# Performance work log

Measured on AMD Instinct MI355X. Metric: run time of the kernel, lower is better.

## Reference

```python
import jax, jax.numpy as jnp
import numpy as np

N_CLASSES = 64
MAX_ITER = 50
EPS = 1e-4


def _sqdist(x, y):
    # squared euclidean distances [n, m]
    d = (x * x).sum(-1)[:, None] + (y * y).sum(-1)[None, :] - 2.0 * (x @ y.T)
    return jnp.maximum(d, 0.0)


def setup_inputs() -> dict:
    key = jax.random.key(0)
    k1, k2, k3 = jax.random.split(key, 3)
    return {
        "feat_s": jax.random.normal(k1, (1600, 1024), jnp.float32),
        "y_s": jax.random.randint(k2, (1600,), 0, N_CLASSES),
        "feat_q": jax.random.normal(k3, (4096, 1024), jnp.float32),
    }


def _prototypes(feat_s, y_s):
    sums = jax.ops.segment_sum(feat_s, y_s, num_segments=N_CLASSES)
    cnt = jax.ops.segment_sum(jnp.ones((feat_s.shape[0],), feat_s.dtype), y_s, num_segments=N_CLASSES)
    return sums / jnp.maximum(cnt, 1.0)[:, None]


def _affinity(feat):
    n = feat.shape[0]
    k = max(1, int(np.log2(n)))  # self-tuning neighborhood size
    dist = jnp.sqrt(_sqdist(feat, feat))
    _, nn_idx = jax.lax.top_k(-dist, k + 1)  # ascending distance order
    rows = jnp.arange(n)
    sigma = dist[rows, nn_idx[:, k]] + 1e-8  # k-th neighbor distance
    nbrs = nn_idx[:, 1:]  # [n, k], drop self
    w = jnp.exp(-jnp.take_along_axis(dist, nbrs, axis=1) / (sigma[:, None] * sigma[nbrs]))
    W = jnp.zeros((n, n), feat.dtype).at[rows[:, None], nbrs].set(w)
    W = (W + W.T) / 2.0
    D_inv = 1.0 / (W.sum(1) + 1e-8)
    return W, D_inv


def _mm_iterations(feat, prototypes, W, D_inv, lam):
    a = _sqdist(feat, prototypes)  # [n, C]
    coef = (lam * D_inv)[:, None]

    def step(y):
        return jax.nn.softmax(-a + coef * (W @ y), axis=1)

    y0 = jax.nn.softmax(-a, axis=1)

    def cond(s):
        y, y_new, i = s
        return (i < MAX_ITER) & (jnp.max(jnp.abs(y_new - y)) >= EPS)

    def body(s):
        y, y_new, i = s
        return (y_new, step(y_new), i + 1)

    y, _, _ = jax.lax.while_loop(cond, body, (y0, step(y0), 0))
    return y


def reference(feat_s, y_s, feat_q):
    protos = _prototypes(feat_s, y_s)
    W, D_inv = _affinity(feat_q)
    d2 = _sqdist(feat_q, protos).min(1)  # squared min distance to prototypes
    d = jnp.sqrt(d2)
    lam = jnp.exp(-d2 / (2.0 * jnp.median(d) ** 2 + 1e-8))
    y = _mm_iterations(feat_q, protos, W, D_inv, lam)
    return jnp.argmax(y, axis=1)
```

## Files before the change

kernel.cpp:

```cpp
#include <hip/hip_runtime.h>
#include <hip/hip_cooperative_groups.h>
#include <cfloat>
#include <cmath>

#define N_Q 4096
#define N_S 1600
#define DIM 1024
#define N_C 64
#define KNN 12
#define MAX_ITER 50
#define EPS_CONV 1e-4f
#define NBLK 256
#define ADJ_CAP 96
#define CHK 256
#define DPAD 40

typedef _Float16 h8 __attribute__((ext_vector_type(8)));
typedef float    f4 __attribute__((ext_vector_type(4)));

__device__ __forceinline__ float wave_max64(float v){
  #pragma unroll
  for (int o = 32; o; o >>= 1) v = fmaxf(v, __shfl_xor(v, o, 64));
  return v;
}
__device__ __forceinline__ float wave_sum64(float v){
  #pragma unroll
  for (int o = 32; o; o >>= 1) v += __shfl_xor(v, o, 64);
  return v;
}
__device__ __forceinline__ float wave_min64(float v){
  #pragma unroll
  for (int o = 32; o; o >>= 1) v = fminf(v, __shfl_xor(v, o, 64));
  return v;
}

__device__ __forceinline__ float aload(const float* p){
  return __hip_atomic_load(p, __ATOMIC_RELAXED, __HIP_MEMORY_SCOPE_AGENT);
}
__device__ __forceinline__ void astore(float* p, float v){
  __hip_atomic_store(p, v, __ATOMIC_RELAXED, __HIP_MEMORY_SCOPE_AGENT);
}
__device__ __forceinline__ int aloadi(const int* p){
  return __hip_atomic_load(p, __ATOMIC_RELAXED, __HIP_MEMORY_SCOPE_AGENT);
}
__device__ __forceinline__ void astorei(int* p, int v){
  __hip_atomic_store(p, v, __ATOMIC_RELAXED, __HIP_MEMORY_SCOPE_AGENT);
}
__device__ __forceinline__ unsigned long long aload64(const unsigned long long* p){
  return __hip_atomic_load(p, __ATOMIC_RELAXED, __HIP_MEMORY_SCOPE_AGENT);
}
__device__ __forceinline__ void astore64(unsigned long long* p, unsigned long long v){
  __hip_atomic_store(p, v, __ATOMIC_RELAXED, __HIP_MEMORY_SCOPE_AGENT);
}

__global__ __launch_bounds__(256) void proto_kernel(
    const float* __restrict__ fs, const int* __restrict__ ys,
    float* __restrict__ Pt, float* __restrict__ pn)
{
  const int c = blockIdx.x, t = threadIdx.x;
  __shared__ int list[N_S];
  __shared__ int pref[256];
  __shared__ int lcount;

  int loc[7]; int cnt = 0;
  const int base = t * 7;
  #pragma unroll
  for (int u = 0; u < 7; u++){
    const int i = base + u;
    if (i < N_S && ys[i] == c) loc[cnt++] = i;
  }
  pref[t] = cnt;
  __syncthreads();
  for (int off = 1; off < 256; off <<= 1){
    int v = (t >= off) ? pref[t - off] : 0;
    __syncthreads();
    pref[t] += v;
    __syncthreads();
  }
  const int start = pref[t] - cnt;
  for (int u = 0; u < cnt; u++) list[start + u] = loc[u];
  if (t == 255) lcount = pref[255];
  __syncthreads();

  const int n = lcount;
  float a0 = 0.f, a1 = 0.f, a2 = 0.f, a3 = 0.f;
  for (int m = 0; m < n; m++){
    const float* r = fs + (size_t)list[m] * DIM;
    a0 += r[t]; a1 += r[t + 256]; a2 += r[t + 512]; a3 += r[t + 768];
  }
  const float inv = 1.0f / fmaxf((float)n, 1.0f);
  const float v0 = a0*inv, v1 = a1*inv, v2 = a2*inv, v3 = a3*inv;
  Pt[(t      )*N_C + c] = v0;
  Pt[(t + 256)*N_C + c] = v1;
  Pt[(t + 512)*N_C + c] = v2;
  Pt[(t + 768)*N_C + c] = v3;
  __shared__ float red[256];
  red[t] = v0*v0 + v1*v1 + v2*v2 + v3*v3;
  __syncthreads();
  for (int o = 128; o; o >>= 1){ if (t < o) red[t] += red[t + o]; __syncthreads(); }
  if (t == 0) pn[c] = red[0];
}

__global__ __launch_bounds__(256) void prep_kernel(
    const float* __restrict__ X, float* __restrict__ qn,
    _Float16* __restrict__ Xh, _Float16* __restrict__ Xl)
{
  const int i = blockIdx.x, t = threadIdx.x;
  const float* r = X + (size_t)i * DIM;
  const float v0 = r[t], v1 = r[t+256], v2 = r[t+512], v3 = r[t+768];
  const size_t b = (size_t)i * DIM;
  _Float16 h0 = (_Float16)v0, h1 = (_Float16)v1, h2 = (_Float16)v2, h3 = (_Float16)v3;
  Xh[b + t      ] = h0; Xl[b + t      ] = (_Float16)(v0 - (float)h0);
  Xh[b + t + 256] = h1; Xl[b + t + 256] = (_Float16)(v1 - (float)h1);
  Xh[b + t + 512] = h2; Xl[b + t + 512] = (_Float16)(v2 - (float)h2);
  Xh[b + t + 768] = h3; Xl[b + t + 768] = (_Float16)(v3 - (float)h3);
  __shared__ float red[256];
  red[t] = v0*v0 + v1*v1 + v2*v2 + v3*v3;
  __syncthreads();
  for (int o = 128; o; o >>= 1){ if (t < o) red[t] += red[t + o]; __syncthreads(); }
  if (t == 0) qn[i] = red[0];
}

__global__ __launch_bounds__(256, 3) void dist_mfma(
    const _Float16* __restrict__ Xh, const _Float16* __restrict__ Xl,
    const float* __restrict__ qn, float* __restrict__ Dq)
{
  __shared__ __align__(16) _Float16 As[2][128][DPAD];
  __shared__ __align__(16) _Float16 Bs[2][128][DPAD];

  const int t = threadIdx.x, w = t >> 6, l = t & 63;
  const int lb  = blockIdx.y * 32 + blockIdx.x;
  const int xcd = lb & 7, k = lb >> 3;
  const int bxs = xcd * 4 + (k >> 5);
  const int bys = k & 31;
  const int bi0 = bys * 128, bj0 = bxs * 128;
  const int i0w = (w >> 1) * 64;
  const int j0w = (w & 1) * 64;
  const int fr = l & 15;
  const int kq = (l >> 4) * 8;

  const int srow = t >> 1;
  const int sseg = (t & 1) * 16;

  f4 acc[4][4];
  #pragma unroll
  for (int a = 0; a < 4; a++)
    #pragma unroll
    for (int b = 0; b < 4; b++) acc[a][b] = (f4){0.f, 0.f, 0.f, 0.f};

  const size_t abase = (size_t)(bi0 + srow) * DIM + sseg;
  const size_t bbase = (size_t)(bj0 + srow) * DIM + sseg;

  #pragma unroll 1
  for (int k0 = 0; k0 < DIM; k0 += 32){
    h8 va0 = *(const h8*)(Xh + abase + k0);
    h8 va1 = *(const h8*)(Xh + abase + k0 + 8);
    h8 vb0 = *(const h8*)(Xl + abase + k0);
    h8 vb1 = *(const h8*)(Xl + abase + k0 + 8);
    h8 vc0 = *(const h8*)(Xh + bbase + k0);
    h8 vc1 = *(const h8*)(Xh + bbase + k0 + 8);
    h8 vd0 = *(const h8*)(Xl + bbase + k0);
    h8 vd1 = *(const h8*)(Xl + bbase + k0 + 8);
    __syncthreads();
    *(h8*)&As[0][srow][sseg    ] = va0;
    *(h8*)&As[0][srow][sseg + 8] = va1;
    *(h8*)&As[1][srow][sseg    ] = vb0;
    *(h8*)&As[1][srow][sseg + 8] = vb1;
    *(h8*)&Bs[0][srow][sseg    ] = vc0;
    *(h8*)&Bs[0][srow][sseg + 8] = vc1;
    *(h8*)&Bs[1][srow][sseg    ] = vd0;
    *(h8*)&Bs[1][srow][sseg + 8] = vd1;
    __syncthreads();

    h8 ah[4], al[4];
    #pragma unroll
    for (int sm = 0; sm < 4; sm++){
      ah[sm] = *(const h8*)&As[0][i0w + sm * 16 + fr][kq];
      al[sm] = *(const h8*)&As[1][i0w + sm * 16 + fr][kq];
    }
    #pragma unroll
    for (int sn = 0; sn < 4; sn++){
      h8 bh = *(const h8*)&Bs[0][j0w + sn * 16 + fr][kq];
      h8 bl = *(const h8*)&Bs[1][j0w + sn * 16 + fr][kq];
      #pragma unroll
      for (int sm = 0; sm < 4; sm++){
        acc[sm][sn] = __builtin_amdgcn_mfma_f32_16x16x32_f16(ah[sm], bh, acc[sm][sn], 0, 0, 0);
        acc[sm][sn] = __builtin_amdgcn_mfma_f32_16x16x32_f16(ah[sm], bl, acc[sm][sn], 0, 0, 0);
        acc[sm][sn] = __builtin_amdgcn_mfma_f32_16x16x32_f16(al[sm], bh, acc[sm][sn], 0, 0, 0);
      }
    }
  }

  const int i0 = bi0 + i0w;
  const int j0 = bj0 + j0w;
  const int cr = (l >> 4) * 4;
  const int cc = l & 15;
  #pragma unroll
  for (int sm = 0; sm < 4; sm++){
    #pragma unroll
    for (int r = 0; r < 4; r++){
      const int row = i0 + sm * 16 + cr + r;
      const float qi = qn[row];
      float* dstrow = &Dq[(size_t)row * N_Q];
      #pragma unroll
      for (int sn = 0; sn < 4; sn++){
        const int col = j0 + sn * 16 + cc;
        float d2 = qi + qn[col] - 2.0f * acc[sm][sn][r];
        dstrow[col] = sqrtf(fmaxf(d2, 0.f));
      }
    }
  }
}

__global__ __launch_bounds__(256) void topk_kernel(
    const float* __restrict__ Dq, int* __restrict__ nbr,
    float* __restrict__ dnbr, float* __restrict__ sigma)
{
  const int i = blockIdx.x, t = threadIdx.x;
  const float* row = Dq + (size_t)i * N_Q;
  float r[16];
  #pragma unroll
  for (int u = 0; u < 16; u++) r[u] = row[t + u * 256];

  __shared__ float pvf[4];
  __shared__ int   pif[4];
  __shared__ int   bwi_s;

  for (int s = 0; s < KNN + 1; s++){
    float best = FLT_MAX; int bj = 0x7fffffff;
    #pragma unroll
    for (int u = 0; u < 16; u++){
      float v = r[u];
      if (v < best){ best = v; bj = t + u * 256; }
    }
    #pragma unroll
    for (int o = 32; o; o >>= 1){
      float ov = __shfl_xor(best, o, 64); int oj = __shfl_xor(bj, o, 64);
      if (ov < best || (ov == best && oj < bj)){ best = ov; bj = oj; }
    }
    if ((t & 63) == 0){ pvf[t >> 6] = best; pif[t >> 6] = bj; }
    __syncthreads();
    if (t == 0){
      float bv = pvf[0]; int bi2 = pif[0];
      #pragma unroll
      for (int w2 = 1; w2 < 4; w2++){
        float v2 = pvf[w2]; int i2 = pif[w2];
        if (v2 < bv || (v2 == bv && i2 < bi2)){ bv = v2; bi2 = i2; }
      }
      bwi_s = bi2;
      if (s >= 1){ nbr[i*KNN + s - 1] = bi2; dnbr[i*KNN + s - 1] = bv; }
      if (s == KNN) sigma[i] = bv + 1e-8f;
    }
    __syncthreads();
    const int widx = bwi_s;
    if ((widx & 255) == t) r[widx >> 8] = FLT_MAX;
  }
}

__device__ __forceinline__ void gbar_leader(int* garr, int* gcnt, int* gen, int target){
  const int g = blockIdx.x >> 4;
  int old = __hip_atomic_fetch_add(&garr[g * 32], 1, __ATOMIC_RELAXED, __HIP_MEMORY_SCOPE_AGENT);
  if ((old & 15) == 15){
    int o2 = __hip_atomic_fetch_add(gcnt, 1, __ATOMIC_RELAXED, __HIP_MEMORY_SCOPE_AGENT);
    if ((o2 & 15) == 15)
      __hip_atomic_fetch_add(gen, 1, __ATOMIC_RELAXED, __HIP_MEMORY_SCOPE_AGENT);
  }
  while (__hip_atomic_load(gen, __ATOMIC_RELAXED, __HIP_MEMORY_SCOPE_AGENT) < target)
    __builtin_amdgcn_s_sleep(1);
}

__device__ __forceinline__ void pbar_wave0(
    unsigned long long* pslot, int ph, int* sdm, float* sdelta_sh, int lane)
{
  const int par = ph & 1;
  unsigned long long* base = pslot + (size_t)par * NBLK;
  if (lane == 0){
    int myd = sdm[par]; sdm[par] = 0;
    unsigned long long pack =
        ((unsigned long long)(unsigned int)myd << 32) | (unsigned int)ph;
    __builtin_amdgcn_s_waitcnt(0);
    astore64(&base[blockIdx.x], pack);
  }
  int mx;
  while (1){
    unsigned long long v0 = aload64(&base[lane      ]);
    unsigned long long v1 = aload64(&base[lane +  64]);
    unsigned long long v2 = aload64(&base[lane + 128]);
    unsigned long long v3 = aload64(&base[lane + 192]);
    int f0 = (int)(unsigned int)v0, f1 = (int)(unsigned int)v1;
    int f2 = (int)(unsigned int)v2, f3 = (int)(unsigned int)v3;
    int mn = f0 < f1 ? f0 : f1;
    mn = f2 < mn ? f2 : mn;
    mn = f3 < mn ? f3 : mn;
    if (__all(mn >= ph)){
      int d0 = (int)(v0 >> 32), d1 = (int)(v1 >> 32);
      int d2 = (int)(v2 >> 32), d3 = (int)(v3 >> 32);
      mx = d0 > d1 ? d0 : d1;
      mx = d2 > mx ? d2 : mx;
      mx = d3 > mx ? d3 : mx;
      break;
    }
    __builtin_amdgcn_s_sleep(1);
  }
  #pragma unroll
  for (int o = 32; o; o >>= 1){ int ox = __shfl_xor(mx, o, 64); mx = ox > mx ? ox : mx; }
  if (lane == 0) *sdelta_sh = __int_as_float(mx);
}

template<int K>
__device__ __forceinline__ void chunk_fma(
    const float* __restrict__ src, const int2* adj, int gbase, int lane,
    float& s0, float& s1, float& s2, float& s3,
    float& s4, float& s5, float& s6, float& s7)
{
  float yv[K][8], wv[K][8];
  #pragma unroll
  for (int g = 0; g < K; g++){
    #pragma unroll
    for (int u = 0; u < 8; u++){
      int2 a = adj[(gbase + g) * 8 + u];
      wv[g][u] = __int_as_float(a.y);
      yv[g][u] = aload(&src[a.x + lane]);
    }
  }
  #pragma unroll
  for (int g = 0; g < K; g++){
    s0 = fmaf(wv[g][0], yv[g][0], s0);
    s1 = fmaf(wv[g][1], yv[g][1], s1);
    s2 = fmaf(wv[g][2], yv[g][2], s2);
    s3 = fmaf(wv[g][3], yv[g][3], s3);
    s4 = fmaf(wv[g][4], yv[g][4], s4);
    s5 = fmaf(wv[g][5], yv[g][5], s5);
    s6 = fmaf(wv[g][6], yv[g][6], s6);
    s7 = fmaf(wv[g][7], yv[g][7], s7);
  }
}

__device__ __forceinline__ float spmv_row(
    const float* __restrict__ src, const int2* adj,
    const int* __restrict__ colA, const float* __restrict__ wA,
    int p0, int p1v, int lane)
{
  const int deg  = p1v - p0;
  const int ncap = deg < ADJ_CAP ? deg : ADJ_CAP;
  const int nfull = ncap & ~7;
  const int ng = nfull >> 3;
  float s0=0.f,s1=0.f,s2=0.f,s3=0.f,s4=0.f,s5=0.f,s6=0.f,s7=0.f;

  int g = 0;
  #pragma unroll 1
  for (; g + 4 <= ng; g += 4){
    chunk_fma<4>(src, adj, g, lane, s0,s1,s2,s3,s4,s5,s6,s7);
  }
  {
    const int left = ng - g;
    if (left == 3)      chunk_fma<3>(src, adj, g, lane, s0,s1,s2,s3,s4,s5,s6,s7);
    else if (left == 2) chunk_fma<2>(src, adj, g, lane, s0,s1,s2,s3,s4,s5,s6,s7);
    else if (left == 1) chunk_fma<1>(src, adj, g, lane, s0,s1,s2,s3,s4,s5,s6,s7);
  }

  if (deg > ADJ_CAP){
    int qg = p0 + ADJ_CAP;
    for (; qg + 8 <= p1v; qg += 8){
      s0 = fmaf(wA[qg    ], aload(&src[colA[qg    ] + lane]), s0);
      s1 = fmaf(wA[qg + 1], aload(&src[colA[qg + 1] + lane]), s1);
      s2 = fmaf(wA[qg + 2], aload(&src[colA[qg + 2] + lane]), s2);
      s3 = fmaf(wA[qg + 3], aload(&src[colA[qg + 3] + lane]), s3);
      s4 = fmaf(wA[qg + 4], aload(&src[colA[qg + 4] + lane]), s4);
      s5 = fmaf(wA[qg + 5], aload(&src[colA[qg + 5] + lane]), s5);
      s6 = fmaf(wA[qg + 6], aload(&src[colA[qg + 6] + lane]), s6);
      s7 = fmaf(wA[qg + 7], aload(&src[colA[qg + 7] + lane]), s7);
    }
    for (; qg < p1v; qg++)
      s0 = fmaf(wA[qg], aload(&src[colA[qg] + lane]), s0);
  } else {
    const int rem = deg - nfull;
    if (rem > 0){
      float yr[7], wr[7];
      #pragma unroll
      for (int u = 0; u < 7; u++){
        if (u < rem){
          int2 a = adj[nfull + u];
          wr[u] = __int_as_float(a.y);
          yr[u] = aload(&src[a.x + lane]);
        }
      }
      #pragma unroll
      for (int u = 0; u < 7; u++)
        if (u < rem) s0 = fmaf(wr[u], yr[u], s0);
    }
  }
  return ((s0+s1)+(s2+s3)) + ((s4+s5)+(s6+s7));
}

__global__ __launch_bounds__(1024, 4) void tail_loop(
    const float* __restrict__ Xq, const float* __restrict__ Pt,
    const float* __restrict__ pn, const float* __restrict__ qn,
    const int* __restrict__ nbr, const float* __restrict__ dnbr,
    const float* __restrict__ sigma,
    float* d2min, float* denom, float* wh,
    float* rowsum, int* indeg, int* rowptr, int* fillc,
    int* colA, float* wA, float* buf0, float* buf1,
    unsigned long long* pslot,
    int* gcnt, int* gen, int* garr, int* __restrict__ out)
{
  __shared__ int   sdm[2];
  __shared__ float sdelta;
  __shared__ union {
    float pchunk[CHK * N_C];
    struct {
      int   ipart[1024];
      int   hist[1024];
      float cand[4096];
      int   candn, b1s, b2s;
    } s;
  } U;
  __shared__ int2  adjL[16 * ADJ_CAP];

  const int tid  = threadIdx.x;
  const int lane = tid & 63;
  const int wv   = tid >> 6;
  const int row  = blockIdx.x * 16 + wv;
  if (tid == 0){ sdm[0] = 0; sdm[1] = 0; }

  const float* xr = Xq + (size_t)row * DIM;
  const f4*    xr4 = (const f4*)xr;
  float dp[8];
  #pragma unroll
  for (int u = 0; u < 8; u++) dp[u] = 0.f;

  for (int f0 = 0; f0 < DIM; f0 += CHK){
    const f4* srcv = (const f4*)(Pt + (size_t)f0 * N_C);
    f4* dstv = (f4*)U.pchunk;
    #pragma unroll
    for (int u = 0; u < 4; u++) dstv[tid + u * 1024] = srcv[tid + u * 1024];
    __syncthreads();
    #pragma unroll 1
    for (int f = 0; f < CHK; f += 8){
      const f4 xa = xr4[(f0 + f) >> 2];
      const f4 xb = xr4[((f0 + f) >> 2) + 1];
      const float* pc = U.pchunk + f * N_C + lane;
      dp[0] = fmaf(xa[0], pc[0      ], dp[0]);
      dp[1] = fmaf(xa[1], pc[N_C    ], dp[1]);
      dp[2] = fmaf(xa[2], pc[N_C * 2], dp[2]);
      dp[3] = fmaf(xa[3], pc[N_C * 3], dp[3]);
      dp[4] = fmaf(xb[0], pc[N_C * 4], dp[4]);
      dp[5] = fmaf(xb[1], pc[N_C * 5], dp[5]);
      dp[6] = fmaf(xb[2], pc[N_C * 6], dp[6]);
      dp[7] = fmaf(xb[3], pc[N_C * 7], dp[7]);
    }
    __syncthreads();
  }
  const float dot = ((dp[0]+dp[1])+(dp[2]+dp[3])) + ((dp[4]+dp[5])+(dp[6]+dp[7]));
  const float av  = fmaxf(qn[row] + pn[lane] - 2.0f * dot, 0.0f);
  const float d2m = wave_min64(av);
  if (lane == 0) astore(&d2min[row], d2m);

  const int e = blockIdx.x * 1024 + tid;
  if (e < N_Q * KNN){
    const int i = e / KNN;
    const int j = nbr[e];
    float wgt = 0.5f * expf(-dnbr[e] / (sigma[i] * sigma[j]));
    astore(&wh[e], wgt);
    atomicAdd(&rowsum[i], wgt);
    atomicAdd(&rowsum[j], wgt);
    atomicAdd(&indeg[j], 1);
  }

  __syncthreads();
  if (tid == 0) gbar_leader(garr, gcnt, gen, 1);
  __syncthreads();

  float xv = -av;
  float m = wave_max64(xv), ee = expf(xv - m), ss = wave_sum64(ee);
  float prev = ee / ss;
  astore(&buf0[row * N_C + lane], prev);

  if (blockIdx.x == 0){
    int* ipart = U.s.ipart;
    const int base = tid * 4;
    int c0 = aloadi(&indeg[base]),     c1 = aloadi(&indeg[base + 1]);
    int c2 = aloadi(&indeg[base + 2]), c3 = aloadi(&indeg[base + 3]);
    const int s4 = c0 + c1 + c2 + c3;
    ipart[tid] = s4;
    __syncthreads();
    for (int off = 1; off < 1024; off <<= 1){
      int v = (tid >= off) ? ipart[tid - off] : 0;
      __syncthreads();
      ipart[tid] += v;
      __syncthreads();
    }
    int run = ipart[tid] - s4;
    astorei(&rowptr[base    ], KNN * (base    ) + run); run += c0;
    astorei(&rowptr[base + 1], KNN * (base + 1) + run); run += c1;
    astorei(&rowptr[base + 2], KNN * (base + 2) + run); run += c2;
    astorei(&rowptr[base + 3], KNN * (base + 3) + run);
    if (tid == 1023) astorei(&rowptr[N_Q], KNN * N_Q + ipart[1023]);
  }
  if (blockIdx.x == 1){
    int*   hist = U.s.hist;
    float* cand = U.s.cand;
    const int base = tid * 4;
    float dv[4];
    #pragma unroll
    for (int u = 0; u < 4; u++) dv[u] = sqrtf(aload(&d2min[base + u]));
    float mn = fminf(fminf(dv[0], dv[1]), fminf(dv[2], dv[3]));
    float mx = fmaxf(fmaxf(dv[0], dv[1]), fmaxf(dv[2], dv[3]));
    mn = wave_min64(mn); mx = wave_max64(mx);
    if (lane == 0){ cand[wv] = mn; cand[wv + 16] = mx; }
    __syncthreads();
    if (tid == 0){
      float a = cand[0], b = cand[16];
      for (int k = 1; k < 16; k++){ a = fminf(a, cand[k]); b = fmaxf(b, cand[16 + k]); }
      cand[32] = a; cand[33] = b;
    }
    __syncthreads();
    mn = cand[32]; mx = cand[33];
    const float rng = mx - mn;
    const float scale = (rng > 0.f) ? (1024.0f / rng) : 0.f;
    hist[tid] = 0;
    __syncthreads();
    int bidx[4];
    #pragma unroll
    for (int u = 0; u < 4; u++){
      int b = (int)((dv[u] - mn) * scale);
      b = b < 0 ? 0 : (b > 1023 ? 1023 : b);
      bidx[u] = b;
      atomicAdd(&hist[b], 1);
    }
    __syncthreads();
    for (int off = 1; off < 1024; off <<= 1){
      int v = (tid >= off) ? hist[tid - off] : 0;
      __syncthreads();
      hist[tid] += v;
      __syncthreads();
    }
    if (hist[tid] >= 2048 && (tid == 0 || hist[tid - 1] < 2048)) U.s.b1s = tid;
    if (hist[tid] >= 2049 && (tid == 0 || hist[tid - 1] < 2049)) U.s.b2s = tid;
    if (tid == 0) U.s.candn = 0;
    __syncthreads();
    const int b1 = U.s.b1s, b2 = U.s.b2s;
    const int cntBefore = (b1 > 0) ? hist[b1 - 1] : 0;
    #pragma unroll
    for (int u = 0; u < 4; u++){
      if (bidx[u] >= b1 && bidx[u] <= b2){
        int pos = atomicAdd(&U.s.candn, 1);
        cand[pos] = dv[u];
      }
    }
    __syncthreads();
    const int mcnt = U.s.candn;
    int P = 2; while (P < mcnt) P <<= 1;
    for (int i2 = mcnt + tid; i2 < P; i2 += 1024) cand[i2] = FLT_MAX;
    __syncthreads();
    for (int k = 2; k <= P; k <<= 1){
      for (int st = k >> 1; st > 0; st >>= 1){
        for (int i2 = tid; i2 < P; i2 += 1024){
          int j2 = i2 ^ st;
          if (j2 > i2){
            float a2 = cand[i2], b3 = cand[j2];
            bool up = ((i2 & k) == 0);
            if (up ? (a2 > b3) : (a2 < b3)){ cand[i2] = b3; cand[j2] = a2; }
          }
        }
        __syncthreads();
      }
    }
    if (tid == 0){
      float v1 = cand[2047 - cntBefore], v2 = cand[2048 - cntBefore];
      float med = 0.5f * (v1 + v2);
      astore(denom, 2.0f * med * med + 1e-8f);
    }
  }

  __syncthreads();
  if (tid == 0) gbar_leader(garr, gcnt, gen, 2);
  __syncthreads();

  if (e < N_Q * KNN){
    const int i = e / KNN, tt = e % KNN;
    const int j = nbr[e];
    const float wgt = aload(&wh[e]);
    const int p = aloadi(&rowptr[i]) + tt;
    colA[p] = j * N_C; wA[p] = wgt;
    const int q = aloadi(&rowptr[j]) + KNN + atomicAdd(&fillc[j], 1);
    colA[q] = i * N_C; wA[q] = wgt;
  }
  const float cf = expf(-d2m / aload(denom)) / (aload(&rowsum[row]) + 1e-8f);
  const int p0  = aloadi(&rowptr[row]);
  const int p1v = aloadi(&rowptr[row + 1]);

  __builtin_amdgcn_fence(__ATOMIC_RELEASE, "agent");
  __syncthreads();
  if (tid == 0) gbar_leader(garr, gcnt, gen, 3);
  __syncthreads();
  __builtin_amdgcn_fence(__ATOMIC_ACQUIRE, "agent");

  {
    const int deg  = p1v - p0;
    const int ncap = deg < ADJ_CAP ? deg : ADJ_CAP;
    for (int u = lane; u < ncap; u += 64)
      adjL[wv * ADJ_CAP + u] = make_int2(colA[p0 + u], __float_as_int(wA[p0 + u]));
  }
  __syncthreads();
  const int2* adj = adjL + wv * ADJ_CAP;

  float cur;
  {
    float sum = spmv_row(buf0, adj, colA, wA, p0, p1v, lane);
    float xv2 = -av + cf * sum;
    float mm = wave_max64(xv2), e2 = expf(xv2 - mm), ss2 = wave_sum64(e2);
    cur = e2 / ss2;
    astore(&buf1[row * N_C + lane], cur);
  }
  float dm = wave_max64(fabsf(cur - prev));
  if (lane == 0) atomicMax(&sdm[1], __float_as_int(dm));
  __syncthreads();
  if (wv == 0) pbar_wave0(pslot, 1, sdm, &sdelta, lane);
  __syncthreads();
  float delta = sdelta;

  int par = 1;
  for (int t = 0;; t++){
    if (t >= MAX_ITER || delta < EPS_CONV) break;
    const float* src = par ? buf1 : buf0;
    float*       dst = par ? buf0 : buf1;
    float sum = spmv_row(src, adj, colA, wA, p0, p1v, lane);
    float xv2 = -av + cf * sum;
    float mm = wave_max64(xv2), e2 = expf(xv2 - mm), ss2 = wave_sum64(e2);
    float nxt = e2 / ss2;
    astore(&dst[row * N_C + lane], nxt);
    const int ph = t + 2;
    dm = wave_max64(fabsf(nxt - cur));
    if (lane == 0) atomicMax(&sdm[ph & 1], __float_as_int(dm));
    __syncthreads();
    if (wv == 0) pbar_wave0(pslot, ph, sdm, &sdelta, lane);
    __syncthreads();
    delta = sdelta;
    prev = cur; cur = nxt; par ^= 1;
  }

  float bv = prev; int bi = lane;
  #pragma unroll
  for (int o = 32; o; o >>= 1){
    float ov = __shfl_xor(bv, o, 64); int oi = __shfl_xor(bi, o, 64);
    if (ov > bv || (ov == bv && oi < bi)){ bv = ov; bi = oi; }
  }
  if (lane == 0) out[row] = bi;
}

extern "C" void kernel_launch(void* const* d_in, const int* in_sizes, int n_in,
                              void* d_out, int out_size, void* d_ws, size_t ws_size,
                              hipStream_t stream)
{
  const float* feat_s = (const float*)d_in[0];
  const int*   y_s    = (const int*)d_in[1];
  const float* feat_q = (const float*)d_in[2];
  int* out = (int*)d_out;

  char* wp = (char*)d_ws;
  auto alloc = [&](size_t bytes) -> char* {
    char* p = wp;
    wp += (bytes + 255) & ~(size_t)255;
    return p;
  };
  float*     Dq  = (float*)alloc((size_t)N_Q * N_Q * 4);
  _Float16*  Xh  = (_Float16*)alloc((size_t)N_Q * DIM * 2);
  _Float16*  Xl  = (_Float16*)alloc((size_t)N_Q * DIM * 2);
  float* Pt     = (float*)alloc((size_t)DIM * N_C * 4);
  float* pn     = (float*)alloc(N_C * 4);
  float* qn     = (float*)alloc(N_Q * 4);
  float* d2min  = (float*)alloc(N_Q * 4);
  float* denom  = (float*)alloc(256);
  int*   nbr    = (int*)alloc((size_t)N_Q * KNN * 4);
  float* dnbr   = (float*)alloc((size_t)N_Q * KNN * 4);
  float* sigma  = (float*)alloc(N_Q * 4);
  float* wh     = (float*)alloc((size_t)N_Q * KNN * 4);
  int*   rowptr = (int*)alloc((N_Q + 1) * 4);
  int*   colA   = (int*)alloc((size_t)2 * N_Q * KNN * 4);
  float* wA     = (float*)alloc((size_t)2 * N_Q * KNN * 4);
  float* buf0   = (float*)alloc((size_t)N_Q * N_C * 4);
  float* buf1   = (float*)alloc((size_t)N_Q * N_C * 4);
  const size_t zbytes = (size_t)N_Q*12 + 256 + 2048 + 2 * NBLK * 8;
  char*  zbase  = alloc(zbytes);
  float* rowsum = (float*)(zbase);
  int*   indeg  = (int*)(zbase + N_Q*4);
  int*   fillc  = (int*)(zbase + N_Q*8);
  int*   syncw  = (int*)(zbase + N_Q*12);
  int*   garr   = (int*)(zbase + N_Q*12 + 256);
  unsigned long long* pslot = (unsigned long long*)(zbase + N_Q*12 + 256 + 2048);

  hipMemsetAsync(zbase, 0, zbytes, stream);

  proto_kernel <<<N_C, 256, 0, stream>>>(feat_s, y_s, Pt, pn);
  prep_kernel  <<<N_Q, 256, 0, stream>>>(feat_q, qn, Xh, Xl);
  dist_mfma    <<<dim3(N_Q/128, N_Q/128), 256, 0, stream>>>(Xh, Xl, qn, Dq);
  topk_kernel  <<<N_Q, 256, 0, stream>>>(Dq, nbr, dnbr, sigma);

  int* gcnt = &syncw[0];
  int* gen  = &syncw[32];
  const float* Xq = feat_q;
  void* args[] = {&Xq, &Pt, &pn, &qn, &nbr, &dnbr, &sigma,
                  &d2min, &denom, &wh, &rowsum, &indeg, &rowptr, &fillc,
                  &colA, &wA, &buf0, &buf1, &pslot,
                  &gcnt, &gen, &garr, &out};
  hipLaunchCooperativeKernel((void*)tail_loop, dim3(NBLK), dim3(1024), args, 0, stream);
}
```

Before: 476.3 us.

## Merge prototype and prep kernels; make top-k selection per-wave without block barriers

Combines the prototype-averaging and query fp16 split/norm kernels into one launch, indexing blocks by role, to remove a launch and let both run concurrently. Rewrites the top-k kernel so each wave independently extracts its own 13 smallest candidates using only shuffles, then one wave merges the 4x13 candidates. This removes the per-step __syncthreads and shared-memory round trips from the 13-step selection loop. The cost is extra candidate storage and a serial merge in a single wave.

```diff
diff --git a/kernel.cpp b/kernel.cpp
--- a/kernel.cpp
+++ b/kernel.cpp
@@ -53,72 +53,77 @@
   __hip_atomic_store(p, v, __ATOMIC_RELAXED, __HIP_MEMORY_SCOPE_AGENT);
 }
 
-__global__ __launch_bounds__(256) void proto_kernel(
+__global__ __launch_bounds__(256) void setup_kernel(
     const float* __restrict__ fs, const int* __restrict__ ys,
-    float* __restrict__ Pt, float* __restrict__ pn)
-{
-  const int c = blockIdx.x, t = threadIdx.x;
-  __shared__ int list[N_S];
-  __shared__ int pref[256];
-  __shared__ int lcount;
-
-  int loc[7]; int cnt = 0;
-  const int base = t * 7;
-  #pragma unroll
-  for (int u = 0; u < 7; u++){
-    const int i = base + u;
-    if (i < N_S && ys[i] == c) loc[cnt++] = i;
-  }
-  pref[t] = cnt;
-  __syncthreads();
-  for (int off = 1; off < 256; off <<= 1){
-    int v = (t >= off) ? pref[t - off] : 0;
-    __syncthreads();
-    pref[t] += v;
-    __syncthreads();
-  }
-  const int start = pref[t] - cnt;
-  for (int u = 0; u < cnt; u++) list[start + u] = loc[u];
-  if (t == 255) lcount = pref[255];
-  __syncthreads();
-
-  const int n = lcount;
-  float a0 = 0.f, a1 = 0.f, a2 = 0.f, a3 = 0.f;
-  for (int m = 0; m < n; m++){
-    const float* r = fs + (size_t)list[m] * DIM;
-    a0 += r[t]; a1 += r[t + 256]; a2 += r[t + 512]; a3 += r[t + 768];
-  }
-  const float inv = 1.0f / fmaxf((float)n, 1.0f);
-  const float v0 = a0*inv, v1 = a1*inv, v2 = a2*inv, v3 = a3*inv;
-  Pt[(t      )*N_C + c] = v0;
-  Pt[(t + 256)*N_C + c] = v1;
-  Pt[(t + 512)*N_C + c] = v2;
-  Pt[(t + 768)*N_C + c] = v3;
-  __shared__ float red[256];
-  red[t] = v0*v0 + v1*v1 + v2*v2 + v3*v3;
-  __syncthreads();
-  for (int o = 128; o; o >>= 1){ if (t < o) red[t] += red[t + o]; __syncthreads(); }
-  if (t == 0) pn[c] = red[0];
-}
-
-__global__ __launch_bounds__(256) void prep_kernel(
+    float* __restrict__ Pt, float* __restrict__ pn,
     const float* __restrict__ X, float* __restrict__ qn,
     _Float16* __restrict__ Xh, _Float16* __restrict__ Xl)
 {
-  const int i = blockIdx.x, t = threadIdx.x;
-  const float* r = X + (size_t)i * DIM;
-  const float v0 = r[t], v1 = r[t+256], v2 = r[t+512], v3 = r[t+768];
-  const size_t b = (size_t)i * DIM;
-  _Float16 h0 = (_Float16)v0, h1 = (_Float16)v1, h2 = (_Float16)v2, h3 = (_Float16)v3;
-  Xh[b + t      ] = h0; Xl[b + t      ] = (_Float16)(v0 - (float)h0);
-  Xh[b + t + 256] = h1; Xl[b + t + 256] = (_Float16)(v1 - (float)h1);
-  Xh[b + t + 512] = h2; Xl[b + t + 512] = (_Float16)(v2 - (float)h2);
-  Xh[b + t + 768] = h3; Xl[b + t + 768] = (_Float16)(v3 - (float)h3);
-  __shared__ float red[256];
-  red[t] = v0*v0 + v1*v1 + v2*v2 + v3*v3;
-  __syncthreads();
-  for (int o = 128; o; o >>= 1){ if (t < o) red[t] += red[t + o]; __syncthreads(); }
-  if (t == 0) qn[i] = red[0];
+  __shared__ union {
+    struct {
+      int   list[N_S];
+      int   pref[256];
+      int   lcount;
+      float red[256];
+    } p;
+    float red[256];
+  } S;
+
+  const int t = threadIdx.x;
+
+  if (blockIdx.x < N_C){
+    const int c = blockIdx.x;
+    int loc[7]; int cnt = 0;
+    const int base = t * 7;
+    #pragma unroll
+    for (int u = 0; u < 7; u++){
+      const int i = base + u;
+      if (i < N_S && ys[i] == c) loc[cnt++] = i;
+    }
+    S.p.pref[t] = cnt;
+    __syncthreads();
+    for (int off = 1; off < 256; off <<= 1){
+      int v = (t >= off) ? S.p.pref[t - off] : 0;
+      __syncthreads();
+      S.p.pref[t] += v;
+      __syncthreads();
+    }
+    const int start = S.p.pref[t] - cnt;
+    for (int u = 0; u < cnt; u++) S.p.list[start + u] = loc[u];
+    if (t == 255) S.p.lcount = S.p.pref[255];
+    __syncthreads();
+
+    const int n = S.p.lcount;
+    float a0 = 0.f, a1 = 0.f, a2 = 0.f, a3 = 0.f;
+    for (int m = 0; m < n; m++){
+      const float* r = fs + (size_t)S.p.list[m] * DIM;
+      a0 += r[t]; a1 += r[t + 256]; a2 += r[t + 512]; a3 += r[t + 768];
+    }
+    const float inv = 1.0f / fmaxf((float)n, 1.0f);
+    const float v0 = a0*inv, v1 = a1*inv, v2 = a2*inv, v3 = a3*inv;
+    Pt[(t      )*N_C + c] = v0;
+    Pt[(t + 256)*N_C + c] = v1;
+    Pt[(t + 512)*N_C + c] = v2;
+    Pt[(t + 768)*N_C + c] = v3;
+    S.p.red[t] = v0*v0 + v1*v1 + v2*v2 + v3*v3;
+    __syncthreads();
+    for (int o = 128; o; o >>= 1){ if (t < o) S.p.red[t] += S.p.red[t + o]; __syncthreads(); }
+    if (t == 0) pn[c] = S.p.red[0];
+  } else {
+    const int i = blockIdx.x - N_C;
+    const float* r = X + (size_t)i * DIM;
+    const float v0 = r[t], v1 = r[t+256], v2 = r[t+512], v3 = r[t+768];
+    const size_t b = (size_t)i * DIM;
+    _Float16 h0 = (_Float16)v0, h1 = (_Float16)v1, h2 = (_Float16)v2, h3 = (_Float16)v3;
+    Xh[b + t      ] = h0; Xl[b + t      ] = (_Float16)(v0 - (float)h0);
+    Xh[b + t + 256] = h1; Xl[b + t + 256] = (_Float16)(v1 - (float)h1);
+    Xh[b + t + 512] = h2; Xl[b + t + 512] = (_Float16)(v2 - (float)h2);
+    Xh[b + t + 768] = h3; Xl[b + t + 768] = (_Float16)(v3 - (float)h3);
+    S.red[t] = v0*v0 + v1*v1 + v2*v2 + v3*v3;
+    __syncthreads();
+    for (int o = 128; o; o >>= 1){ if (t < o) S.red[t] += S.red[t + o]; __syncthreads(); }
+    if (t == 0) qn[i] = S.red[0];
+  }
 }
 
 __global__ __launch_bounds__(256, 3) void dist_mfma(
@@ -217,15 +222,16 @@
     float* __restrict__ dnbr, float* __restrict__ sigma)
 {
   const int i = blockIdx.x, t = threadIdx.x;
+  const int lane = t & 63, w = t >> 6;
   const float* row = Dq + (size_t)i * N_Q;
   float r[16];
   #pragma unroll
   for (int u = 0; u < 16; u++) r[u] = row[t + u * 256];
 
-  __shared__ float pvf[4];
-  __shared__ int   pif[4];
-  __shared__ int   bwi_s;
-
+  __shared__ float cvf[4 * (KNN + 1)];
+  __shared__ int   cif[4 * (KNN + 1)];
+
+  float keepv = FLT_MAX; int keepi = 0x7fffffff;
   for (int s = 0; s < KNN + 1; s++){
     float best = FLT_MAX; int bj = 0x7fffffff;
     #pragma unroll
@@ -238,22 +244,28 @@
       float ov = __shfl_xor(best, o, 64); int oj = __shfl_xor(bj, o, 64);
       if (ov < best || (ov == best && oj < bj)){ best = ov; bj = oj; }
     }
-    if ((t & 63) == 0){ pvf[t >> 6] = best; pif[t >> 6] = bj; }
-    __syncthreads();
-    if (t == 0){
-      float bv = pvf[0]; int bi2 = pif[0];
+    if (lane == s){ keepv = best; keepi = bj; }
+    if ((bj & 255) == t) r[bj >> 8] = FLT_MAX;
+  }
+  if (lane < KNN + 1){ cvf[w * (KNN + 1) + lane] = keepv; cif[w * (KNN + 1) + lane] = keepi; }
+  __syncthreads();
+
+  if (w == 0){
+    float mv = FLT_MAX; int mi = 0x7fffffff;
+    if (lane < 4 * (KNN + 1)){ mv = cvf[lane]; mi = cif[lane]; }
+    for (int s = 0; s < KNN + 1; s++){
+      float best = mv; int bj = mi;
       #pragma unroll
-      for (int w2 = 1; w2 < 4; w2++){
-        float v2 = pvf[w2]; int i2 = pif[w2];
-        if (v2 < bv || (v2 == bv && i2 < bi2)){ bv = v2; bi2 = i2; }
+      for (int o = 32; o; o >>= 1){
+        float ov = __shfl_xor(best, o, 64); int oj = __shfl_xor(bj, o, 64);
+        if (ov < best || (ov == best && oj < bj)){ best = ov; bj = oj; }
       }
-      bwi_s = bi2;
-      if (s >= 1){ nbr[i*KNN + s - 1] = bi2; dnbr[i*KNN + s - 1] = bv; }
-      if (s == KNN) sigma[i] = bv + 1e-8f;
-    }
-    __syncthreads();
-    const int widx = bwi_s;
-    if ((widx & 255) == t) r[widx >> 8] = FLT_MAX;
+      if (lane == 0){
+        if (s >= 1){ nbr[i*KNN + s - 1] = bj; dnbr[i*KNN + s - 1] = best; }
+        if (s == KNN) sigma[i] = best + 1e-8f;
+      }
+      if (mi == bj) mv = FLT_MAX;
+    }
   }
 }
 
@@ -692,8 +704,7 @@
 
   hipMemsetAsync(zbase, 0, zbytes, stream);
 
-  proto_kernel <<<N_C, 256, 0, stream>>>(feat_s, y_s, Pt, pn);
-  prep_kernel  <<<N_Q, 256, 0, stream>>>(feat_q, qn, Xh, Xl);
+  setup_kernel <<<N_Q + N_C, 256, 0, stream>>>(feat_s, y_s, Pt, pn, feat_q, qn, Xh, Xl);
   dist_mfma    <<<dim3(N_Q/128, N_Q/128), 256, 0, stream>>>(Xh, Xl, qn, Dq);
   topk_kernel  <<<N_Q, 256, 0, stream>>>(Dq, nbr, dnbr, sigma);
 
```

New measurement: 472.6 us. No clear change (-0.8%).
